# Optimization experiments

Hardware: AMD Instinct MI355X
Metric: run time of the kernel (lower is better)

Reference implementation:

```python
import jax, jax.numpy as jnp
import numpy as np

B, T, E, H = 4, 2048, 1024, 16
D = E // H

def setup_inputs() -> dict:
    key = jax.random.key(0)
    ks = jax.random.split(key, 8)
    s = 0.02
    return {
        "q": jax.random.normal(ks[0], (B, T, E), dtype=jnp.float32),
        "k": jax.random.normal(ks[1], (B, T, E), dtype=jnp.float32),
        "v": jax.random.normal(ks[2], (B, T, E), dtype=jnp.float32),
        "Wq": jax.random.normal(ks[3], (E, E), dtype=jnp.float32) * s,
        "Wk": jax.random.normal(ks[4], (E, E), dtype=jnp.float32) * s,
        "Wv": jax.random.normal(ks[5], (E, E), dtype=jnp.float32) * s,
        "Wp": jax.random.normal(ks[6], (E, E), dtype=jnp.float32) * s,
        "bp": jnp.zeros((E,), dtype=jnp.float32),
    }

def reference(q, k, v, Wq, Wk, Wv, Wp, bp):
    # Linear projections (torch Linear: x @ W.T). NOTE: original code computes
    # key from the already-projected query (k = self.key(q)); external k is unused.
    qp = q @ Wq.T                      # [B,T,E]
    kp = qp @ Wk.T                     # [B,T,E]  <- faithful quirk
    vp = v @ Wv.T                      # [B,T,E]
    qh = qp.reshape(B, T, H, D).transpose(0, 2, 1, 3)  # [B,H,T,D]
    kh = kp.reshape(B, T, H, D).transpose(0, 2, 1, 3)
    vh = vp.reshape(B, T, H, D).transpose(0, 2, 1, 3)
    # Faithful quirk: att = scores / D**(-1/2) == scores * sqrt(D)
    scale = jnp.float32(D) ** 0.5
    att = jnp.einsum('bhtd,bhsd->bhts', qh, kh) * scale  # [B,H,T,T]
    causal = jnp.tril(jnp.ones((T, T), dtype=bool))
    att = jnp.where(causal, att, -jnp.inf)
    att = jax.nn.softmax(att, axis=-1)
    y = jnp.einsum('bhts,bhsd->bhtd', att, vh)           # [B,H,T,D]
    y = y.transpose(0, 2, 1, 3).reshape(B, T, E)
    return y @ Wp.T + bp
```

## Files before the change

kernel.cpp:

```cpp
#include <hip/hip_runtime.h>


typedef unsigned short u16;
typedef unsigned int   u32;
typedef __attribute__((ext_vector_type(8))) __bf16 bf16x8;
typedef __attribute__((ext_vector_type(8))) u16    u16x8;
typedef __attribute__((ext_vector_type(4))) u16    u16x4;
typedef __attribute__((ext_vector_type(4))) float  f32x4;
typedef __attribute__((ext_vector_type(4))) int    i32x4;

#define DEV static __device__ __forceinline__

DEV u16 f2bf(float x){ union{float f;u32 u;}v; v.f=x; u32 r=v.u+0x7fffu+((v.u>>16)&1u); return (u16)(r>>16); }
DEV float bf2f(u16 b){ union{u32 u;float f;}v; v.u=((u32)b)<<16; return v.f; }
DEV f32x4 zero4(){ f32x4 z={0.f,0.f,0.f,0.f}; return z; }
DEV f32x4 mfma16(bf16x8 a, bf16x8 b, f32x4 c){ return __builtin_amdgcn_mfma_f32_16x16x32_bf16(a,b,c,0,0,0); }
DEV void gld16(const u16* g, u16* l){
  __builtin_amdgcn_global_load_lds((const __attribute__((address_space(1))) u32*)g,
                                   (__attribute__((address_space(3))) u32*)l, 16, 0, 0);
}
DEV u32 pkbf(float a, float b){
  union{float f;u32 u;}x,y; x.f=a; y.f=b;
  return __builtin_amdgcn_perm(y.u+0x8000u, x.u+0x8000u, 0x07060302u);
}

constexpr int B_=4, T_=2048, E_=1024;
constexpr int M_=B_*T_;
constexpr float L2E8 = 11.5415603f;

__global__ __launch_bounds__(256)
void cvt_a(const float* __restrict__ q, const float* __restrict__ v,
           u16* __restrict__ qi, u16* __restrict__ vb)
{
  const int j=blockIdx.y;
  const size_t e=((size_t)blockIdx.x*256+threadIdx.x)*8;
  const float* s=(j==0)?q:v;
  f32x4 x0=*reinterpret_cast<const f32x4*>(s+e);
  f32x4 x1=*reinterpret_cast<const f32x4*>(s+e+4);
  u16x8 h,l;
#pragma unroll
  for(int t=0;t<4;t++){
    u16 hh=f2bf(x0[t]); h[t]=hh; l[t]=f2bf(x0[t]-bf2f(hh));
    u16 h2=f2bf(x1[t]); h[t+4]=h2; l[t+4]=f2bf(x1[t]-bf2f(h2));
  }
  if(j==0){
    const size_t row=e>>10, k=e&1023;
    u16* d=qi + row*2048 + (k>>3)*16;
    *reinterpret_cast<u16x8*>(d)=h;
    *reinterpret_cast<u16x8*>(d+8)=l;
  } else {
    *reinterpret_cast<u16x8*>(vb+e)=h;
  }
}

__global__ __launch_bounds__(256)
void cvt_w(const float* __restrict__ Wq, const float* __restrict__ Wk, const float* __restrict__ Wv,
           u16* __restrict__ wqi, u16* __restrict__ wki, u16* __restrict__ wvb)
{
  const int j=blockIdx.y;
  const size_t e=((size_t)blockIdx.x*256+threadIdx.x)*8;
  const float* s=(j==0)?Wq:(j==1)?Wk:Wv;
  f32x4 x0=*reinterpret_cast<const f32x4*>(s+e);
  f32x4 x1=*reinterpret_cast<const f32x4*>(s+e+4);
  u16x8 h,l;
#pragma unroll
  for(int t=0;t<4;t++){
    u16 hh=f2bf(x0[t]); h[t]=hh; l[t]=f2bf(x0[t]-bf2f(hh));
    u16 h2=f2bf(x1[t]); h[t+4]=h2; l[t+4]=f2bf(x1[t]-bf2f(h2));
  }
  if(j==2){ *reinterpret_cast<u16x8*>(wvb+e)=h; return; }
  u16* base=(j==0)?wqi:wki;
  const size_t row=e>>10, k=e&1023;
  u16* d=base + row*2048 + (k>>3)*16;
  *reinterpret_cast<u16x8*>(d)=h;
  *reinterpret_cast<u16x8*>(d+8)=l;
}

template<int SPLIT,int WF32,int OMODE>
__global__ __launch_bounds__(256)
void gemm(const u16* __restrict__ Ag, const u16* __restrict__ Bg,
          const float* __restrict__ Wf, const float* __restrict__ bias,
          u16* __restrict__ Ob, float* __restrict__ Of)
{
  __shared__ u16 sA[128*64];
  __shared__ u16 sB[WF32 ? 128*68 : 128*64];

  const int tid=threadIdx.x, wave=tid>>6, lane=tid&63;
  const int quad=lane>>4, l16=lane&15, sw=l16&7;
  const int wm=(wave>>1)*64, wn=(wave&1)*64;
  const int n0=blockIdx.x*128, m0=blockIdx.y*128;
  constexpr int KSTEP = SPLIT?32:64;

  f32x4 acc[4][4];
#pragma unroll
  for(int i=0;i<4;i++)
#pragma unroll
    for(int j=0;j<4;j++) acc[i][j]=zero4();

  for(int k0=0;k0<E_;k0+=KSTEP){
#pragma unroll
    for(int it=0;it<4;it++){
      const int c=it*256+tid, row=c>>3, j=(c&7)^(row&7);
      const u16* ga = SPLIT ? Ag + (size_t)(m0+row)*2048 + (size_t)(k0>>3)*16 + j*8
                            : Ag + (size_t)(m0+row)*1024 + k0 + j*8;
      gld16(ga, &sA[(it*256+wave*64)*8]);
    }
    if(!WF32){
#pragma unroll
      for(int it=0;it<4;it++){
        const int c=it*256+tid, row=c>>3, j=(c&7)^(row&7);
        const u16* gb = SPLIT ? Bg + (size_t)(n0+row)*2048 + (size_t)(k0>>3)*16 + j*8
                              : Bg + (size_t)(n0+row)*1024 + k0 + j*8;
        gld16(gb, &sB[(it*256+wave*64)*8]);
      }
    } else {
#pragma unroll
      for(int it=0;it<8;it++){
        const int idx=it*256+tid, row=idx>>4, col=(idx&15)*4;
        f32x4 w=*reinterpret_cast<const f32x4*>(Wf + (size_t)(n0+row)*1024 + k0+col);
        u16x4 hh;
#pragma unroll
        for(int t=0;t<4;t++) hh[t]=f2bf(w[t]);
        *reinterpret_cast<u16x4*>(&sB[row*68+col])=hh;
      }
    }
    __syncthreads();

    if(SPLIT){
      bf16x8 ahh[4],ahl[4],bhh[4],bhl[4];
#pragma unroll
      for(int i=0;i<4;i++){
        const u16* pa=&sA[(wm+i*16+l16)*64];
        const u16* pb=&sB[(wn+i*16+l16)*64];
        ahh[i]=*reinterpret_cast<const bf16x8*>(&pa[((2*quad  )^sw)*8]);
        ahl[i]=*reinterpret_cast<const bf16x8*>(&pa[((2*quad+1)^sw)*8]);
        bhh[i]=*reinterpret_cast<const bf16x8*>(&pb[((2*quad  )^sw)*8]);
        bhl[i]=*reinterpret_cast<const bf16x8*>(&pb[((2*quad+1)^sw)*8]);
      }
#pragma unroll
      for(int i=0;i<4;i++)
#pragma unroll
        for(int j=0;j<4;j++){
          acc[i][j]=mfma16(ahh[i],bhh[j],acc[i][j]);
          acc[i][j]=mfma16(ahh[i],bhl[j],acc[i][j]);
          acc[i][j]=mfma16(ahl[i],bhh[j],acc[i][j]);
        }
    } else {
#pragma unroll
      for(int kk=0;kk<2;kk++){
        bf16x8 a[4],b[4];
#pragma unroll
        for(int i=0;i<4;i++){
          a[i]=*reinterpret_cast<const bf16x8*>(&sA[(wm+i*16+l16)*64 + (((kk*4+quad)^sw)*8)]);
          b[i]= WF32 ? *reinterpret_cast<const bf16x8*>(&sB[(wn+i*16+l16)*68 + kk*32+quad*8])
                     : *reinterpret_cast<const bf16x8*>(&sB[(wn+i*16+l16)*64 + (((kk*4+quad)^sw)*8)]);
        }
#pragma unroll
        for(int i=0;i<4;i++)
#pragma unroll
          for(int j=0;j<4;j++)
            acc[i][j]=mfma16(a[i],b[j],acc[i][j]);
      }
    }
    __syncthreads();
  }

#pragma unroll
  for(int i=0;i<4;i++)
#pragma unroll
    for(int j=0;j<4;j++){
      const int col=n0+wn+j*16+l16;
#pragma unroll
      for(int r=0;r<4;r++){
        const int row=m0+wm+i*16+quad*4+r;
        float v=acc[i][j][r];
        if(OMODE==2)      Of[(size_t)row*E_+col]=v+bias[col];
        else if(OMODE==1) Ob[(size_t)row*E_+col]=f2bf(v);
        else {
          u16 hh=f2bf(v);
          const size_t base=(size_t)row*2048 + (size_t)(col>>3)*16 + (col&7);
          Ob[base]=hh; Ob[base+8]=f2bf(v-bf2f(hh));
        }
      }
    }
}

__global__ __launch_bounds__(256)
void attn(const u16* __restrict__ qpi, const u16* __restrict__ kpi,
          const u16* __restrict__ vph, u16* __restrict__ yout)
{
  constexpr int VP=68;
  __shared__ u16 sK[64*128];
  __shared__ u16 sV[64*VP];

  const int tid=threadIdx.x, wave=tid>>6, lane=tid&63;
  const int quad=lane>>4, l16=lane&15, sw=l16&7;
  const int qt=(int)(gridDim.x-1-blockIdx.x)>>6;
  const int bh=blockIdx.x&63;
  const int b=bh>>4, h=bh&15;
  const int qr0=qt*128+wave*32;

  bf16x8 qfh[2][2], qfl[2][2];
#pragma unroll
  for(int mt=0;mt<2;mt++)
#pragma unroll
    for(int ksv=0;ksv<2;ksv++){
      const size_t off=(size_t)(b*T_+qr0+mt*16+l16)*2048 + h*128 + (ksv*4+quad)*16;
      qfh[mt][ksv]=*reinterpret_cast<const bf16x8*>(qpi+off);
      qfl[mt][ksv]=*reinterpret_cast<const bf16x8*>(qpi+off+8);
    }

  float mst[2]={-1e30f,-1e30f}, lst[2]={0.f,0.f};
  f32x4 oacc[2][4];
#pragma unroll
  for(int mt=0;mt<2;mt++)
#pragma unroll
    for(int dt=0;dt<4;dt++) oacc[mt][dt]=zero4();

  const int nkt=2*(qt+1);
  for(int kt=0;kt<nkt;kt++){
    const int s0=kt*64;
    __syncthreads();
#pragma unroll
    for(int it=0;it<4;it++){
      const int c=it*256+tid, row=c>>4, j=(c&15)^(row&7);
      gld16(kpi + (size_t)(b*T_+s0+row)*2048 + h*128 + j*8,
            &sK[(it*256+wave*64)*8]);
    }
#pragma unroll
    for(int it=0;it<2;it++){
      const int c=it*256+tid, s=c&63, dc=(c>>6)*8;
      u16x8 vv=*reinterpret_cast<const u16x8*>(vph + (size_t)(b*T_+s0+s)*1024 + h*64 + dc);
#pragma unroll
      for(int j=0;j<8;j++) sV[(dc+j)*VP+s]=vv[j];
    }
    __syncthreads();

    if(s0<=qr0+31){
      f32x4 sacc[4][2];
#pragma unroll
      for(int st=0;st<4;st++)
#pragma unroll
        for(int mt=0;mt<2;mt++) sacc[st][mt]=zero4();
#pragma unroll
      for(int st=0;st<4;st++)
#pragma unroll
        for(int ksv=0;ksv<2;ksv++){
          const u16* pk=&sK[(st*16+l16)*128];
          bf16x8 kh=*reinterpret_cast<const bf16x8*>(&pk[((2*(ksv*4+quad)  )^sw)*8]);
          bf16x8 kl=*reinterpret_cast<const bf16x8*>(&pk[((2*(ksv*4+quad)+1)^sw)*8]);
#pragma unroll
          for(int mt=0;mt<2;mt++){
            sacc[st][mt]=mfma16(kh,qfh[mt][ksv],sacc[st][mt]);
            sacc[st][mt]=mfma16(kl,qfh[mt][ksv],sacc[st][mt]);
            sacc[st][mt]=mfma16(kh,qfl[mt][ksv],sacc[st][mt]);
          }
        }
      const bool needmask=(s0+63>qr0);
      u32 pk_[4][2][2];
#pragma unroll
      for(int mt=0;mt<2;mt++){
        const int qrow=qr0+mt*16+l16;
        float mloc=-1e30f;
#pragma unroll
        for(int st=0;st<4;st++)
#pragma unroll
          for(int r=0;r<4;r++){
            float v=sacc[st][mt][r];
            if(needmask && (s0+st*16+quad*4+r>qrow)) v=-1e30f;
            sacc[st][mt][r]=v;
            mloc=fmaxf(mloc,v);
          }
        mloc=fmaxf(mloc,__shfl_xor(mloc,16,64));
        mloc=fmaxf(mloc,__shfl_xor(mloc,32,64));
        const float nm=fmaxf(mst[mt],mloc);
        const float alpha=exp2f((mst[mt]-nm)*L2E8);
        mst[mt]=nm;
        const float cexp=nm*L2E8;
        float rs=0.f;
#pragma unroll
        for(int st=0;st<4;st++)
#pragma unroll
          for(int r=0;r<4;r++){
            float p=exp2f(__builtin_fmaf(sacc[st][mt][r],L2E8,-cexp));
            sacc[st][mt][r]=p;
            rs+=p;
          }
        rs+=__shfl_xor(rs,16,64);
        rs+=__shfl_xor(rs,32,64);
        lst[mt]=lst[mt]*alpha+rs;
#pragma unroll
        for(int dt=0;dt<4;dt++) oacc[mt][dt]*=alpha;
#pragma unroll
        for(int st=0;st<4;st++){
          pk_[st][mt][0]=pkbf(sacc[st][mt][0],sacc[st][mt][1]);
          pk_[st][mt][1]=pkbf(sacc[st][mt][2],sacc[st][mt][3]);
        }
      }
      const int srcA=(2*(quad&1))*16+l16, srcB=srcA+16;
      const bool hs=(quad>=2);
#pragma unroll
      for(int ksv=0;ksv<2;ksv++){
        bf16x8 b2[2];
#pragma unroll
        for(int mt=0;mt<2;mt++){
          int e0=__shfl((int)pk_[2*ksv  ][mt][0],srcA,64);
          int g0=__shfl((int)pk_[2*ksv+1][mt][0],srcA,64);
          int e1=__shfl((int)pk_[2*ksv  ][mt][1],srcA,64);
          int g1=__shfl((int)pk_[2*ksv+1][mt][1],srcA,64);
          int e2=__shfl((int)pk_[2*ksv  ][mt][0],srcB,64);
          int g2=__shfl((int)pk_[2*ksv+1][mt][0],srcB,64);
          int e3=__shfl((int)pk_[2*ksv  ][mt][1],srcB,64);
          int g3=__shfl((int)pk_[2*ksv+1][mt][1],srcB,64);
          i32x4 bd={ hs?g0:e0, hs?g1:e1, hs?g2:e2, hs?g3:e3 };
          b2[mt]=*reinterpret_cast<bf16x8*>(&bd);
        }
#pragma unroll
        for(int dt=0;dt<4;dt++){
          bf16x8 va=*reinterpret_cast<const bf16x8*>(&sV[(dt*16+l16)*VP+ksv*32+quad*8]);
#pragma unroll
          for(int mt=0;mt<2;mt++)
            oacc[mt][dt]=mfma16(va,b2[mt],oacc[mt][dt]);
        }
      }
    }
  }
#pragma unroll
  for(int mt=0;mt<2;mt++){
    const float inv=1.0f/lst[mt];
    const size_t rb=(size_t)(b*T_+qr0+mt*16+l16)*1024 + h*64;
#pragma unroll
    for(int dt=0;dt<4;dt++){
      u16x4 o4;
#pragma unroll
      for(int r=0;r<4;r++) o4[r]=f2bf(oacc[mt][dt][r]*inv);
      *reinterpret_cast<u16x4*>(yout + rb + dt*16 + quad*4)=o4;
    }
  }
}

extern "C" void kernel_launch(void* const* d_in, const int* in_sizes, int n_in,
                              void* d_out, int out_size, void* d_ws, size_t ws_size,
                              hipStream_t stream)
{
  const float* q =(const float*)d_in[0];
  const float* v =(const float*)d_in[2];
  const float* Wq=(const float*)d_in[3];
  const float* Wk=(const float*)d_in[4];
  const float* Wv=(const float*)d_in[5];
  const float* Wp=(const float*)d_in[6];
  const float* bp=(const float*)d_in[7];
  float* out=(float*)d_out;

  const size_t NE=(size_t)M_*E_;
  const size_t WE=(size_t)E_*E_;
  u16* wsv=(u16*)d_ws;
  u16* qsl_i=wsv;
  u16* qp_i =wsv+2*NE;
  u16* kp_i =wsv;
  u16* vpb  =wsv+4*NE;
  u16* ybf  =wsv+5*NE;
  u16* og   =(u16*)d_out;
  u16* wq_i =og;
  u16* wk_i =og+2*WE;
  u16* wv_b =og+4*WE;
  u16* vb   =og+5*WE;

  dim3 blk(256);
  cvt_a<<<dim3(NE/2048,2), blk, 0, stream>>>(q, v, qsl_i, vb);
  cvt_w<<<dim3(WE/2048,3), blk, 0, stream>>>(Wq, Wk, Wv, wq_i, wk_i, wv_b);

  dim3 g(E_/128, M_/128);
  gemm<1,0,0><<<g, blk, 0, stream>>>(qsl_i, wq_i, nullptr, nullptr, qp_i, nullptr);
  gemm<1,0,0><<<g, blk, 0, stream>>>(qp_i,  wk_i, nullptr, nullptr, kp_i, nullptr);
  gemm<0,0,1><<<g, blk, 0, stream>>>(vb,    wv_b, nullptr, nullptr, vpb,  nullptr);
  attn<<<dim3(1024), blk, 0, stream>>>(qp_i, kp_i, vpb, ybf);
  gemm<0,1,2><<<g, blk, 0, stream>>>(ybf, nullptr, Wp, bp, nullptr, out);
}
```

Before: 459.9 us.

## Produce transposed V projection, pre-convert Wp, widen split GEMM K-step

The V projection GEMM now swaps its operands so it writes V already transposed (d-major), which lets the attention kernel load V tiles with async global-to-LDS copies instead of scalar transposing LDS stores. Wp is converted to bf16 once by a new kernel, so the output GEMM no longer converts fp32 on the fly. The split-precision GEMM now processes 64 K per iteration with larger LDS tiles, halving the number of barriers. The softmax row-sum lane reduction is also deferred to the end of the attention kernel. The trade-offs are an extra kernel launch and higher LDS use in the split GEMM, which may lower occupancy.

After: 428.1 us. -6.9%, faster.

```diff
diff --git a/kernel.cpp b/kernel.cpp
--- a/kernel.cpp
+++ b/kernel.cpp
@@ -76,20 +76,31 @@
   *reinterpret_cast<u16x8*>(d+8)=l;
 }
 
-template<int SPLIT,int WF32,int OMODE>
+__global__ __launch_bounds__(256)
+void cvt_p(const float* __restrict__ Wp, u16* __restrict__ wpb)
+{
+  const size_t e=((size_t)blockIdx.x*256+threadIdx.x)*8;
+  f32x4 x0=*reinterpret_cast<const f32x4*>(Wp+e);
+  f32x4 x1=*reinterpret_cast<const f32x4*>(Wp+e+4);
+  u16x8 h;
+#pragma unroll
+  for(int t=0;t<4;t++){ h[t]=f2bf(x0[t]); h[t+4]=f2bf(x1[t]); }
+  *reinterpret_cast<u16x8*>(wpb+e)=h;
+}
+
+template<int SPLIT,int OMODE>
 __global__ __launch_bounds__(256)
 void gemm(const u16* __restrict__ Ag, const u16* __restrict__ Bg,
-          const float* __restrict__ Wf, const float* __restrict__ bias,
-          u16* __restrict__ Ob, float* __restrict__ Of)
-{
-  __shared__ u16 sA[128*64];
-  __shared__ u16 sB[WF32 ? 128*68 : 128*64];
+          const float* __restrict__ bias,
+          u16* __restrict__ Ob, float* __restrict__ Of, int ldc)
+{
+  __shared__ u16 sA[SPLIT?128*128:128*64];
+  __shared__ u16 sB[SPLIT?128*128:128*64];
 
   const int tid=threadIdx.x, wave=tid>>6, lane=tid&63;
   const int quad=lane>>4, l16=lane&15, sw=l16&7;
   const int wm=(wave>>1)*64, wn=(wave&1)*64;
   const int n0=blockIdx.x*128, m0=blockIdx.y*128;
-  constexpr int KSTEP = SPLIT?32:64;
 
   f32x4 acc[4][4];
 #pragma unroll
@@ -97,63 +108,60 @@
 #pragma unroll
     for(int j=0;j<4;j++) acc[i][j]=zero4();
 
-  for(int k0=0;k0<E_;k0+=KSTEP){
-#pragma unroll
-    for(int it=0;it<4;it++){
-      const int c=it*256+tid, row=c>>3, j=(c&7)^(row&7);
-      const u16* ga = SPLIT ? Ag + (size_t)(m0+row)*2048 + (size_t)(k0>>3)*16 + j*8
-                            : Ag + (size_t)(m0+row)*1024 + k0 + j*8;
-      gld16(ga, &sA[(it*256+wave*64)*8]);
-    }
-    if(!WF32){
+  for(int k0=0;k0<E_;k0+=64){
+    if(SPLIT){
+#pragma unroll
+      for(int it=0;it<8;it++){
+        const int c=it*256+tid, row=c>>4, j=(c&15)^(row&7);
+        gld16(Ag + (size_t)(m0+row)*2048 + k0*2 + j*8, &sA[(it*256+wave*64)*8]);
+      }
+#pragma unroll
+      for(int it=0;it<8;it++){
+        const int c=it*256+tid, row=c>>4, j=(c&15)^(row&7);
+        gld16(Bg + (size_t)(n0+row)*2048 + k0*2 + j*8, &sB[(it*256+wave*64)*8]);
+      }
+    } else {
 #pragma unroll
       for(int it=0;it<4;it++){
         const int c=it*256+tid, row=c>>3, j=(c&7)^(row&7);
-        const u16* gb = SPLIT ? Bg + (size_t)(n0+row)*2048 + (size_t)(k0>>3)*16 + j*8
-                              : Bg + (size_t)(n0+row)*1024 + k0 + j*8;
-        gld16(gb, &sB[(it*256+wave*64)*8]);
-      }
-    } else {
-#pragma unroll
-      for(int it=0;it<8;it++){
-        const int idx=it*256+tid, row=idx>>4, col=(idx&15)*4;
-        f32x4 w=*reinterpret_cast<const f32x4*>(Wf + (size_t)(n0+row)*1024 + k0+col);
-        u16x4 hh;
-#pragma unroll
-        for(int t=0;t<4;t++) hh[t]=f2bf(w[t]);
-        *reinterpret_cast<u16x4*>(&sB[row*68+col])=hh;
+        gld16(Ag + (size_t)(m0+row)*1024 + k0 + j*8, &sA[(it*256+wave*64)*8]);
+      }
+#pragma unroll
+      for(int it=0;it<4;it++){
+        const int c=it*256+tid, row=c>>3, j=(c&7)^(row&7);
+        gld16(Bg + (size_t)(n0+row)*1024 + k0 + j*8, &sB[(it*256+wave*64)*8]);
       }
     }
     __syncthreads();
 
-    if(SPLIT){
-      bf16x8 ahh[4],ahl[4],bhh[4],bhl[4];
-#pragma unroll
-      for(int i=0;i<4;i++){
-        const u16* pa=&sA[(wm+i*16+l16)*64];
-        const u16* pb=&sB[(wn+i*16+l16)*64];
-        ahh[i]=*reinterpret_cast<const bf16x8*>(&pa[((2*quad  )^sw)*8]);
-        ahl[i]=*reinterpret_cast<const bf16x8*>(&pa[((2*quad+1)^sw)*8]);
-        bhh[i]=*reinterpret_cast<const bf16x8*>(&pb[((2*quad  )^sw)*8]);
-        bhl[i]=*reinterpret_cast<const bf16x8*>(&pb[((2*quad+1)^sw)*8]);
-      }
-#pragma unroll
-      for(int i=0;i<4;i++)
-#pragma unroll
-        for(int j=0;j<4;j++){
-          acc[i][j]=mfma16(ahh[i],bhh[j],acc[i][j]);
-          acc[i][j]=mfma16(ahh[i],bhl[j],acc[i][j]);
-          acc[i][j]=mfma16(ahl[i],bhh[j],acc[i][j]);
-        }
-    } else {
-#pragma unroll
-      for(int kk=0;kk<2;kk++){
+#pragma unroll
+    for(int kk=0;kk<2;kk++){
+      if(SPLIT){
+        bf16x8 ahh[4],ahl[4],bhh[4],bhl[4];
+#pragma unroll
+        for(int i=0;i<4;i++){
+          const u16* pa=&sA[(wm+i*16+l16)*128];
+          const u16* pb=&sB[(wn+i*16+l16)*128];
+          const int ch=2*(kk*4+quad);
+          ahh[i]=*reinterpret_cast<const bf16x8*>(&pa[((ch  )^sw)*8]);
+          ahl[i]=*reinterpret_cast<const bf16x8*>(&pa[((ch+1)^sw)*8]);
+          bhh[i]=*reinterpret_cast<const bf16x8*>(&pb[((ch  )^sw)*8]);
+          bhl[i]=*reinterpret_cast<const bf16x8*>(&pb[((ch+1)^sw)*8]);
+        }
+#pragma unroll
+        for(int i=0;i<4;i++)
+#pragma unroll
+          for(int j=0;j<4;j++){
+            acc[i][j]=mfma16(ahh[i],bhh[j],acc[i][j]);
+            acc[i][j]=mfma16(ahh[i],bhl[j],acc[i][j]);
+            acc[i][j]=mfma16(ahl[i],bhh[j],acc[i][j]);
+          }
+      } else {
         bf16x8 a[4],b[4];
 #pragma unroll
         for(int i=0;i<4;i++){
           a[i]=*reinterpret_cast<const bf16x8*>(&sA[(wm+i*16+l16)*64 + (((kk*4+quad)^sw)*8)]);
-          b[i]= WF32 ? *reinterpret_cast<const bf16x8*>(&sB[(wn+i*16+l16)*68 + kk*32+quad*8])
-                     : *reinterpret_cast<const bf16x8*>(&sB[(wn+i*16+l16)*64 + (((kk*4+quad)^sw)*8)]);
+          b[i]=*reinterpret_cast<const bf16x8*>(&sB[(wn+i*16+l16)*64 + (((kk*4+quad)^sw)*8)]);
         }
 #pragma unroll
         for(int i=0;i<4;i++)
@@ -174,8 +182,8 @@
       for(int r=0;r<4;r++){
         const int row=m0+wm+i*16+quad*4+r;
         float v=acc[i][j][r];
-        if(OMODE==2)      Of[(size_t)row*E_+col]=v+bias[col];
-        else if(OMODE==1) Ob[(size_t)row*E_+col]=f2bf(v);
+        if(OMODE==2)      Of[(size_t)row*ldc+col]=v+bias[col];
+        else if(OMODE==1) Ob[(size_t)row*ldc+col]=f2bf(v);
         else {
           u16 hh=f2bf(v);
           const size_t base=(size_t)row*2048 + (size_t)(col>>3)*16 + (col&7);
@@ -187,11 +195,10 @@
 
 __global__ __launch_bounds__(256)
 void attn(const u16* __restrict__ qpi, const u16* __restrict__ kpi,
-          const u16* __restrict__ vph, u16* __restrict__ yout)
-{
-  constexpr int VP=68;
-  __shared__ u16 sK[64*128];
-  __shared__ u16 sV[64*VP];
+          const u16* __restrict__ vpT, u16* __restrict__ yout)
+{
+  __shared__ u16 sK [64*128];
+  __shared__ u16 sVT[64*64];
 
   const int tid=threadIdx.x, wave=tid>>6, lane=tid&63;
   const int quad=lane>>4, l16=lane&15, sw=l16&7;
@@ -229,10 +236,9 @@
     }
 #pragma unroll
     for(int it=0;it<2;it++){
-      const int c=it*256+tid, s=c&63, dc=(c>>6)*8;
-      u16x8 vv=*reinterpret_cast<const u16x8*>(vph + (size_t)(b*T_+s0+s)*1024 + h*64 + dc);
-#pragma unroll
-      for(int j=0;j<8;j++) sV[(dc+j)*VP+s]=vv[j];
+      const int c=it*256+tid, row=c>>3, j=(c&7)^(row&7);
+      gld16(vpT + (size_t)(h*64+row)*8192 + b*T_ + s0 + j*8,
+            &sVT[(it*256+wave*64)*8]);
     }
     __syncthreads();
 
@@ -247,8 +253,9 @@
 #pragma unroll
         for(int ksv=0;ksv<2;ksv++){
           const u16* pk=&sK[(st*16+l16)*128];
-          bf16x8 kh=*reinterpret_cast<const bf16x8*>(&pk[((2*(ksv*4+quad)  )^sw)*8]);
-          bf16x8 kl=*reinterpret_cast<const bf16x8*>(&pk[((2*(ksv*4+quad)+1)^sw)*8]);
+          const int ch=2*(ksv*4+quad);
+          bf16x8 kh=*reinterpret_cast<const bf16x8*>(&pk[((ch  )^sw)*8]);
+          bf16x8 kl=*reinterpret_cast<const bf16x8*>(&pk[((ch+1)^sw)*8]);
 #pragma unroll
           for(int mt=0;mt<2;mt++){
             sacc[st][mt]=mfma16(kh,qfh[mt][ksv],sacc[st][mt]);
@@ -286,8 +293,6 @@
             sacc[st][mt][r]=p;
             rs+=p;
           }
-        rs+=__shfl_xor(rs,16,64);
-        rs+=__shfl_xor(rs,32,64);
         lst[mt]=lst[mt]*alpha+rs;
 #pragma unroll
         for(int dt=0;dt<4;dt++) oacc[mt][dt]*=alpha;
@@ -317,7 +322,7 @@
         }
 #pragma unroll
         for(int dt=0;dt<4;dt++){
-          bf16x8 va=*reinterpret_cast<const bf16x8*>(&sV[(dt*16+l16)*VP+ksv*32+quad*8]);
+          bf16x8 va=*reinterpret_cast<const bf16x8*>(&sVT[(dt*16+l16)*64 + (((ksv*4+quad)^sw)*8)]);
 #pragma unroll
           for(int mt=0;mt<2;mt++)
             oacc[mt][dt]=mfma16(va,b2[mt],oacc[mt][dt]);
@@ -327,7 +332,10 @@
   }
 #pragma unroll
   for(int mt=0;mt<2;mt++){
-    const float inv=1.0f/lst[mt];
+    float lt=lst[mt];
+    lt+=__shfl_xor(lt,16,64);
+    lt+=__shfl_xor(lt,32,64);
+    const float inv=1.0f/lt;
     const size_t rb=(size_t)(b*T_+qr0+mt*16+l16)*1024 + h*64;
 #pragma unroll
     for(int dt=0;dt<4;dt++){
@@ -358,7 +366,8 @@
   u16* qsl_i=wsv;
   u16* qp_i =wsv+2*NE;
   u16* kp_i =wsv;
-  u16* vpb  =wsv+4*NE;
+  u16* wp_b =wsv+2*NE;
+  u16* vpT  =wsv+4*NE;
   u16* ybf  =wsv+5*NE;
   u16* og   =(u16*)d_out;
   u16* wq_i =og;
@@ -371,9 +380,10 @@
   cvt_w<<<dim3(WE/2048,3), blk, 0, stream>>>(Wq, Wk, Wv, wq_i, wk_i, wv_b);
 
   dim3 g(E_/128, M_/128);
-  gemm<1,0,0><<<g, blk, 0, stream>>>(qsl_i, wq_i, nullptr, nullptr, qp_i, nullptr);
-  gemm<1,0,0><<<g, blk, 0, stream>>>(qp_i,  wk_i, nullptr, nullptr, kp_i, nullptr);
-  gemm<0,0,1><<<g, blk, 0, stream>>>(vb,    wv_b, nullptr, nullptr, vpb,  nullptr);
-  attn<<<dim3(1024), blk, 0, stream>>>(qp_i, kp_i, vpb, ybf);
-  gemm<0,1,2><<<g, blk, 0, stream>>>(ybf, nullptr, Wp, bp, nullptr, out);
-}
+  gemm<1,0><<<g, blk, 0, stream>>>(qsl_i, wq_i, nullptr, qp_i, nullptr, 0);
+  gemm<1,0><<<g, blk, 0, stream>>>(qp_i, wk_i, nullptr, kp_i, nullptr, 0);
+  gemm<0,1><<<dim3(M_/128, E_/128), blk, 0, stream>>>(wv_b, vb, nullptr, vpT, nullptr, M_);
+  attn<<<dim3(1024), blk, 0, stream>>>(qp_i, kp_i, vpT, ybf);
+  cvt_p<<<dim3(WE/2048), blk, 0, stream>>>(Wp, wp_b);
+  gemm<0,2><<<g, blk, 0, stream>>>(ybf, wp_b, bp, nullptr, out, E_);
+}
```
